# Kernel optimization log

Hardware: AMD Instinct MI355X
Metric: run time of the kernel (lower is better)

## Reference

```python
import jax, jax.numpy as jnp
import numpy as np

B, T, D, H, L, V = 4, 1024, 1024, 16, 12, 8192
DH = D // H
FF = 4 * D


def _ln(x, g, b, eps=1e-5):
    m = x.mean(-1, keepdims=True)
    v = x.var(-1, keepdims=True)
    return (x - m) / jnp.sqrt(v + eps) * g + b


def setup_inputs() -> dict:
    key = jax.random.key(0)
    ks = iter(jax.random.split(key, 32))
    s = 0.02
    inp = {
        "idx": jax.random.randint(next(ks), (B, T), 0, V),
        "tk_emb": jax.random.normal(next(ks), (V, D), jnp.float32) * s,
        "pos_emb": jax.random.normal(next(ks), (V, D), jnp.float32) * s,
        "ln1_g": jnp.ones((L, D)), "ln1_b": jnp.zeros((L, D)),
        "Wq": jax.random.normal(next(ks), (L, H, D, DH), jnp.float32) * s,
        "bq": jnp.zeros((L, H, DH)),
        "Wk": jax.random.normal(next(ks), (L, H, D, DH), jnp.float32) * s,
        "bk": jnp.zeros((L, H, DH)),
        "Wv": jax.random.normal(next(ks), (L, H, D, DH), jnp.float32) * s,
        "bv": jnp.zeros((L, H, DH)),
        "Wo": jax.random.normal(next(ks), (L, D, D), jnp.float32) * s,
        "bo": jnp.zeros((L, D)),
        "ln2_g": jnp.ones((L, D)), "ln2_b": jnp.zeros((L, D)),
        "W1": jax.random.normal(next(ks), (L, D, FF), jnp.float32) * s,
        "b1": jnp.zeros((L, FF)),
        "W2": jax.random.normal(next(ks), (L, FF, D), jnp.float32) * s,
        "b2": jnp.zeros((L, D)),
        "lnf_g": jnp.ones((D,)), "lnf_b": jnp.zeros((D,)),
        "Wout": jax.random.normal(next(ks), (D, V), jnp.float32) * s,
        "bout": jnp.zeros((V,)),
    }
    return inp


def reference(idx, tk_emb, pos_emb, ln1_g, ln1_b, Wq, bq, Wk, bk, Wv, bv,
              Wo, bo, ln2_g, ln2_b, W1, b1, W2, b2, lnf_g, lnf_b, Wout, bout):
    b, t = idx.shape
    x = tk_emb[idx] + pos_emb[:t][None]          # [B,T,D]
    causal = jnp.tril(jnp.ones((t, t), bool))    # [T,T]
    scale = 1.0 / jnp.sqrt(jnp.asarray(DH, x.dtype))

    def block(x, p):
        g1, b1_, wq, bq_, wk, bk_, wv, bv_, wo, bo_, g2, b2_, w1, bb1, w2, bb2 = p
        h = _ln(x, g1, b1_)
        q = jnp.einsum('btd,hde->bhte', h, wq) + bq_[:, None, :]
        k = jnp.einsum('btd,hde->bhte', h, wk) + bk_[:, None, :]
        v = jnp.einsum('btd,hde->bhte', h, wv) + bv_[:, None, :]
        scores = jnp.einsum('bhte,bhse->bhts', q, k) * scale
        scores = jnp.where(causal, scores, jnp.asarray(-jnp.inf, scores.dtype))
        att = jax.nn.softmax(scores, axis=-1)
        o = jnp.einsum('bhts,bhse->bhte', att, v)              # [B,H,T,dh]
        o = o.transpose(0, 2, 1, 3).reshape(x.shape[0], x.shape[1], -1)
        x = x + o @ wo + bo_
        h2 = _ln(x, g2, b2_)
        x = x + jax.nn.gelu(h2 @ w1 + bb1, approximate=False) @ w2 + bb2
        return x, None

    layer_params = (ln1_g, ln1_b, Wq, bq, Wk, bk, Wv, bv, Wo, bo,
                    ln2_g, ln2_b, W1, b1, W2, b2)
    x, _ = jax.lax.scan(block, x, layer_params)
    x = _ln(x, lnf_g, lnf_b)
    logits = x @ Wout + bout
    return logits
```

## Files before the change

### kernel.cpp

```cpp
#include <hip/hip_runtime.h>

#define B_ 4
#define T_ 1024
#define D_ 1024
#define H_ 16
#define DH_ 64
#define L_ 12
#define FF_ 4096
#define V_ 8192
#define M_ 4096

typedef short bf16x8 __attribute__((ext_vector_type(8)));
typedef unsigned short u16x8 __attribute__((ext_vector_type(8)));
typedef unsigned short u16x4 __attribute__((ext_vector_type(4)));
typedef float f32x4 __attribute__((ext_vector_type(4)));

typedef const __attribute__((address_space(1))) void* gas1;
typedef __attribute__((address_space(3))) void* las3;
#define GL2LDS(g, l) __builtin_amdgcn_global_load_lds((gas1)(g), (las3)(l), 16, 0, 0)
#define MFMA16(a, b, c) __builtin_amdgcn_mfma_f32_16x16x32_bf16((a), (b), (c), 0, 0, 0)
#define WVM(n) asm volatile("s_waitcnt vmcnt(" #n ")" ::: "memory")
#define BARRIER() asm volatile("s_barrier" ::: "memory")

static __device__ __forceinline__ unsigned short f2bf(float f) {
  unsigned int u = __builtin_bit_cast(unsigned int, f);
  u += 0x7fffu + ((u >> 16) & 1u);
  return (unsigned short)(u >> 16);
}

__global__ __launch_bounds__(256) void embed_kernel(const int* __restrict__ idx,
                                                    const float* __restrict__ tk,
                                                    const float* __restrict__ pe,
                                                    float* __restrict__ x) {
  const int row = blockIdx.x;
  const int t = row & (T_ - 1);
  const int id = idx[row];
  const int c = threadIdx.x * 4;
  float4 a = *(const float4*)&tk[(size_t)id * D_ + c];
  const float4 p = *(const float4*)&pe[(size_t)t * D_ + c];
  a.x += p.x; a.y += p.y; a.z += p.z; a.w += p.w;
  *(float4*)&x[(size_t)row * D_ + c] = a;
}

__global__ __launch_bounds__(256) void ln_kernel(const float* __restrict__ x,
                                                 const float* __restrict__ g,
                                                 const float* __restrict__ bb,
                                                 unsigned short* __restrict__ out) {
  __shared__ float red[8];
  const int row = blockIdx.x, tid = threadIdx.x;
  const float4 v = *(const float4*)&x[(size_t)row * D_ + tid * 4];
  float s = v.x + v.y + v.z + v.w;
  float s2 = v.x * v.x + v.y * v.y + v.z * v.z + v.w * v.w;
#pragma unroll
  for (int off = 32; off; off >>= 1) {
    s += __shfl_down(s, off);
    s2 += __shfl_down(s2, off);
  }
  if ((tid & 63) == 0) { red[tid >> 6] = s; red[4 + (tid >> 6)] = s2; }
  __syncthreads();
  const float ts = red[0] + red[1] + red[2] + red[3];
  const float ts2 = red[4] + red[5] + red[6] + red[7];
  const float mean = ts * (1.f / 1024.f);
  const float var = ts2 * (1.f / 1024.f) - mean * mean;
  const float rstd = rsqrtf(var + 1e-5f);
  const int c = tid * 4;
  u16x4 ov;
  ov[0] = f2bf((v.x - mean) * rstd * g[c] + bb[c]);
  ov[1] = f2bf((v.y - mean) * rstd * g[c + 1] + bb[c + 1]);
  ov[2] = f2bf((v.z - mean) * rstd * g[c + 2] + bb[c + 2]);
  ov[3] = f2bf((v.w - mean) * rstd * g[c + 3] + bb[c + 3]);
  *(u16x4*)&out[(size_t)row * D_ + c] = ov;
}

__global__ __launch_bounds__(256) void tpose_kernel(const float* __restrict__ in,
                                                    unsigned short* __restrict__ out,
                                                    int R, int C, long in_bs,
                                                    long out_bs_i, int inner, long out_bs_o) {
  __shared__ float tile[32][33];
  const int z = blockIdx.z;
  in += (long)z * in_bs;
  out += (long)(z % inner) * out_bs_i + (long)(z / inner) * out_bs_o;
  const int tx = threadIdx.x, ty = threadIdx.y;
  const int c = blockIdx.x * 32 + tx;
  const int r = blockIdx.y * 32 + ty;
#pragma unroll
  for (int i = 0; i < 4; i++) tile[ty + i * 8][tx] = in[(long)(r + i * 8) * C + c];
  __syncthreads();
  const int oc = blockIdx.y * 32 + tx;
  const int orr = blockIdx.x * 32 + ty;
#pragma unroll
  for (int i = 0; i < 4; i++) out[(long)(orr + i * 8) * R + oc] = f2bf(tile[tx][ty + i * 8]);
}

__global__ void bcat_kernel(const float* __restrict__ bq, const float* __restrict__ bk,
                            const float* __restrict__ bv, float* __restrict__ bqkv) {
  const int l = blockIdx.x;
  for (int i = threadIdx.x; i < 1024; i += 256) {
    bqkv[l * 3072 + i] = bq[l * 1024 + i];
    bqkv[l * 3072 + 1024 + i] = bk[l * 1024 + i];
    bqkv[l * 3072 + 2048 + i] = bv[l * 1024 + i];
  }
}

__global__ __launch_bounds__(256) void redk_kernel(const float* __restrict__ part,
                                                   const float* __restrict__ bias,
                                                   float* __restrict__ x, int N) {
  const size_t i = ((size_t)blockIdx.x * 256 + threadIdx.x) * 4;
  const int col = (int)(i & (size_t)(N - 1));
  float4 r = *(const float4*)&x[i];
  const float4 bv = *(const float4*)&bias[col];
  const size_t stride = (size_t)M_ * N;
  float4 p0 = *(const float4*)&part[i];
  float4 p1 = *(const float4*)&part[i + stride];
  float4 p2 = *(const float4*)&part[i + 2 * stride];
  float4 p3 = *(const float4*)&part[i + 3 * stride];
  r.x += bv.x + ((p0.x + p1.x) + (p2.x + p3.x));
  r.y += bv.y + ((p0.y + p1.y) + (p2.y + p3.y));
  r.z += bv.z + ((p0.z + p1.z) + (p2.z + p3.z));
  r.w += bv.w + ((p0.w + p1.w) + (p2.w + p3.w));
  *(float4*)&x[i] = r;
}

template <int EPI>
__global__ __launch_bounds__(512, 2) void gemm256(const unsigned short* __restrict__ A,
                                                  const unsigned short* __restrict__ Bt,
                                                  const float* __restrict__ bias,
                                                  void* outp, int Kc, int ld, int N) {
  __shared__ unsigned short lds[65536];
  const int tid = threadIdx.x;
  const int lane = tid & 63, w = tid >> 6;
  const int wm = w >> 2, wn = w & 3;
  const int l15 = lane & 15, lh = lane >> 4;
  const int row0 = blockIdx.y * 256, col0 = blockIdx.x * 256;
  const int z = blockIdx.z;
  const int nt = Kc >> 6;
  const int laneoff = (lh * 8) ^ (((l15 >> 1) & 3) << 3);
  const int cswz = ((tid & 3) * 8) ^ (((tid >> 3) & 3) << 3);
  const unsigned short* gA = A + (size_t)(row0 + (tid >> 2)) * ld + z * Kc + cswz;
  const unsigned short* gB = Bt + (size_t)(col0 + (tid >> 2)) * ld + z * Kc + cswz;
  const size_t rblk = (size_t)128 * ld;
  const int arow = wm * 128 + l15;
  const int brow = wn * 64 + l15;

  f32x4 acc[8][4];
#pragma unroll
  for (int m = 0; m < 8; m++)
#pragma unroll
    for (int n = 0; n < 4; n++) acc[m][n] = f32x4{0.f, 0.f, 0.f, 0.f};

  auto issueA = [&](int t, int r) {
    unsigned short* d = lds + (t & 1) * 32768 + r * 8192 + tid * 8;
    const unsigned short* s = gA + t * 64 + r * 32;
    GL2LDS(s, d);
    GL2LDS(s + rblk, d + 4096);
  };
  auto issueB = [&](int t, int r) {
    unsigned short* d = lds + (t & 1) * 32768 + 16384 + r * 8192 + tid * 8;
    const unsigned short* s = gB + t * 64 + r * 32;
    GL2LDS(s, d);
    GL2LDS(s + rblk, d + 4096);
  };

  issueA(0, 0); issueB(0, 0); issueA(0, 1); issueB(0, 1);
  issueA(1, 0); issueB(1, 0);
  WVM(8);
  BARRIER();

  bf16x8 aF[4], bF[4];
  for (int t = 0; t < nt; ++t) {
    const bool last = (t == nt - 1);
    const unsigned short* ab = lds + (t & 1) * 32768;
    const unsigned short* bb2 = ab + 16384;
#pragma unroll
    for (int m = 0; m < 4; m++) aF[m] = *(const bf16x8*)(ab + (arow + m * 16) * 32 + laneoff);
#pragma unroll
    for (int n = 0; n < 4; n++) bF[n] = *(const bf16x8*)(bb2 + (brow + n * 16) * 32 + laneoff);
    if (!last) issueA(t + 1, 1);
    BARRIER();
    __builtin_amdgcn_s_setprio(1);
#pragma unroll
    for (int m = 0; m < 4; m++)
#pragma unroll
      for (int n = 0; n < 4; n++) acc[m][n] = MFMA16(aF[m], bF[n], acc[m][n]);
    __builtin_amdgcn_s_setprio(0);
    BARRIER();
#pragma unroll
    for (int m = 0; m < 4; m++) aF[m] = *(const bf16x8*)(ab + (arow + (m + 4) * 16) * 32 + laneoff);
    if (!last) issueB(t + 1, 1);
    BARRIER();
    __builtin_amdgcn_s_setprio(1);
#pragma unroll
    for (int m = 0; m < 4; m++)
#pragma unroll
      for (int n = 0; n < 4; n++) acc[m + 4][n] = MFMA16(aF[m], bF[n], acc[m + 4][n]);
    __builtin_amdgcn_s_setprio(0);
    if (last) { WVM(0); } else { WVM(8); }
    BARRIER();
#pragma unroll
    for (int m = 0; m < 4; m++) aF[m] = *(const bf16x8*)(ab + 8192 + (arow + m * 16) * 32 + laneoff);
#pragma unroll
    for (int n = 0; n < 4; n++) bF[n] = *(const bf16x8*)(bb2 + 8192 + (brow + n * 16) * 32 + laneoff);
    if (t + 2 < nt) issueA(t + 2, 0);
    BARRIER();
    __builtin_amdgcn_s_setprio(1);
#pragma unroll
    for (int m = 0; m < 4; m++)
#pragma unroll
      for (int n = 0; n < 4; n++) acc[m][n] = MFMA16(aF[m], bF[n], acc[m][n]);
    __builtin_amdgcn_s_setprio(0);
    BARRIER();
#pragma unroll
    for (int m = 0; m < 4; m++) aF[m] = *(const bf16x8*)(ab + 8192 + (arow + (m + 4) * 16) * 32 + laneoff);
    if (t + 2 < nt) issueB(t + 2, 0);
    BARRIER();
    __builtin_amdgcn_s_setprio(1);
#pragma unroll
    for (int m = 0; m < 4; m++)
#pragma unroll
      for (int n = 0; n < 4; n++) acc[m + 4][n] = MFMA16(aF[m], bF[n], acc[m + 4][n]);
    __builtin_amdgcn_s_setprio(0);
    if (!last) {
      if (t == nt - 2) { WVM(4); } else { WVM(8); }
    }
    BARRIER();
  }

#pragma unroll
  for (int n = 0; n < 4; n++) {
    const int c = col0 + wn * 64 + n * 16 + l15;
    const float bv = (EPI == 4) ? 0.f : bias[c];
#pragma unroll
    for (int m = 0; m < 8; m++) {
      const int r = row0 + wm * 128 + m * 16 + lh * 4;
#pragma unroll
      for (int j = 0; j < 4; j++) {
        float val = acc[m][n][j] + bv;
        const size_t oi = (size_t)(r + j) * N + c;
        if constexpr (EPI == 0) {
          ((unsigned short*)outp)[oi] = f2bf(val);
        } else if constexpr (EPI == 1) {
          val = 0.5f * val * (1.f + erff(val * 0.70710678118654752f));
          ((unsigned short*)outp)[oi] = f2bf(val);
        } else if constexpr (EPI == 4) {
          ((float*)outp)[(size_t)z * ((size_t)gridDim.y * 256) * N + oi] = val;
        } else {
          ((float*)outp)[oi] = val;
        }
      }
    }
  }
}

template <int EPI, int BN, int DEPTH>
__global__ __launch_bounds__(256) void gemmP(const unsigned short* __restrict__ A,
                                             const unsigned short* __restrict__ Bt,
                                             const float* __restrict__ bias,
                                             const float* resid, void* outp,
                                             int K, int N) {
  constexpr int NB = DEPTH + 1;
  constexpr int TILE = (128 + BN) * 32;
  constexpr int NF = BN / 32;
  __shared__ unsigned short lds[NB * TILE];
  const int tid = threadIdx.x;
  const int lane = tid & 63;
  const int w = tid >> 6;
  const int l15 = lane & 15, lh = lane >> 4;
  const int wr = (w >> 1) * 64, wc = (w & 1) * (BN / 2);
  const int row0 = blockIdx.y * 128, col0 = blockIdx.x * BN;

  const unsigned short* gA = A + (size_t)(row0 + (tid >> 2)) * K + (tid & 3) * 8;
  const unsigned short* gB = Bt + (size_t)(col0 + (tid >> 2)) * K + (tid & 3) * 8;
  const size_t rstep = (size_t)64 * K;

  f32x4 acc[4][NF];
#pragma unroll
  for (int m = 0; m < 4; m++)
#pragma unroll
    for (int n = 0; n < NF; n++) acc[m][n] = f32x4{0.f, 0.f, 0.f, 0.f};

  const int nt = K >> 5;

  auto ISSUE = [&](int t) {
    unsigned short* buf = lds + (t % NB) * TILE;
    const unsigned short* a = gA + t * 32;
    GL2LDS(a, buf + tid * 8);
    GL2LDS(a + rstep, buf + 2048 + tid * 8);
    const unsigned short* b = gB + t * 32;
    unsigned short* bb = buf + 128 * 32;
    GL2LDS(b, bb + tid * 8);
    if constexpr (BN == 128) GL2LDS(b + rstep, bb + 2048 + tid * 8);
  };

#pragma unroll
  for (int t = 0; t < DEPTH; t++) ISSUE(t);

  for (int i = 0; i < nt; i++) {
    const int rem = nt - 1 - i;
    if (rem >= DEPTH - 1) {
      if constexpr ((2 + (BN == 128 ? 2 : 1)) * (DEPTH - 1) == 4) WVM(4);
      else WVM(6);
    } else if (DEPTH == 3 && rem == 1) {
      WVM(3);
    } else {
      WVM(0);
    }
    BARRIER();
    const unsigned short* buf = lds + (i % NB) * TILE;
    const unsigned short* rdA = buf + (wr + l15) * 32 + lh * 8;
    const unsigned short* rdB = buf + 128 * 32 + (wc + l15) * 32 + lh * 8;
    bf16x8 aF[4], bF[NF];
#pragma unroll
    for (int m = 0; m < 4; m++) aF[m] = *(const bf16x8*)(rdA + m * 512);
#pragma unroll
    for (int n = 0; n < NF; n++) bF[n] = *(const bf16x8*)(rdB + n * 512);
#pragma unroll
    for (int m = 0; m < 4; m++)
#pragma unroll
      for (int n = 0; n < NF; n++) acc[m][n] = MFMA16(aF[m], bF[n], acc[m][n]);
    if (i + DEPTH < nt) ISSUE(i + DEPTH);
  }

#pragma unroll
  for (int n = 0; n < NF; n++) {
    const int c = col0 + wc + n * 16 + l15;
    const float bv = bias[c];
#pragma unroll
    for (int m = 0; m < 4; m++) {
      const int r = row0 + wr + m * 16 + lh * 4;
#pragma unroll
      for (int j = 0; j < 4; j++) {
        float val = acc[m][n][j] + bv;
        const size_t oi = (size_t)(r + j) * N + c;
        if constexpr (EPI == 0) {
          ((unsigned short*)outp)[oi] = f2bf(val);
        } else if constexpr (EPI == 1) {
          val = 0.5f * val * (1.f + erff(val * 0.70710678118654752f));
          ((unsigned short*)outp)[oi] = f2bf(val);
        } else if constexpr (EPI == 2) {
          ((float*)outp)[oi] = resid[oi] + val;
        } else {
          ((float*)outp)[oi] = val;
        }
      }
    }
  }
}

__global__ __launch_bounds__(256) void attn_kernel(const unsigned short* __restrict__ qkv,
                                                   unsigned short* __restrict__ o) {
  __shared__ unsigned short Ks[64 * 72];
  __shared__ unsigned short Vts[64 * 72];
  __shared__ unsigned short Ps[4][16 * 72];
  const int tid = threadIdx.x;
  const int lane = tid & 63, w = tid >> 6;
  const int l15 = lane & 15, lh = lane >> 4;
  const int qt = blockIdx.x;
  const int bh = blockIdx.y;
  const int b = bh >> 4, h = bh & 15;
  const int rb = b * T_;
  const int q0 = qt * 64;

  bf16x8 qf[2];
  {
    const unsigned short* qp = qkv + (size_t)(rb + q0 + w * 16 + l15) * 3072 + h * 64 + lh * 8;
    qf[0] = *(const bf16x8*)qp;
    qf[1] = *(const bf16x8*)(qp + 32);
  }
  f32x4 oa[4];
  float mrun[4], lrun[4];
#pragma unroll
  for (int n = 0; n < 4; n++) oa[n] = f32x4{0.f, 0.f, 0.f, 0.f};
#pragma unroll
  for (int j = 0; j < 4; j++) { mrun[j] = -1e30f; lrun[j] = 0.f; }

  const int row_l = w * 16 + lh * 4;

  for (int kt = 0; kt <= qt; ++kt) {
    __syncthreads();
#pragma unroll
    for (int p = 0; p < 2; p++) {
      const int cc = tid + p * 256;
      const int s = cc >> 3, e8 = (cc & 7) * 8;
      *(u16x8*)&Ks[s * 72 + e8] =
          *(const u16x8*)(qkv + (size_t)(rb + kt * 64 + s) * 3072 + 1024 + h * 64 + e8);
    }
    {
      const unsigned short* vp =
          qkv + (size_t)(rb + kt * 64 + lane) * 3072 + 2048 + h * 64 + w * 16;
      const u16x8 v0 = *(const u16x8*)vp;
      const u16x8 v1 = *(const u16x8*)(vp + 8);
#pragma unroll
      for (int j = 0; j < 8; j++) Vts[(w * 16 + j) * 72 + lane] = v0[j];
#pragma unroll
      for (int j = 0; j < 8; j++) Vts[(w * 16 + 8 + j) * 72 + lane] = v1[j];
    }
    __syncthreads();

    f32x4 sa[4];
#pragma unroll
    for (int n = 0; n < 4; n++) sa[n] = f32x4{0.f, 0.f, 0.f, 0.f};
#pragma unroll
    for (int ke = 0; ke < 2; ke++) {
#pragma unroll
      for (int n = 0; n < 4; n++) {
        const bf16x8 kf = *(const bf16x8*)&Ks[(n * 16 + l15) * 72 + ke * 32 + lh * 8];
        sa[n] = MFMA16(qf[ke], kf, sa[n]);
      }
    }
    float sv[4][4];
    const bool diag = (kt == qt);
#pragma unroll
    for (int n = 0; n < 4; n++) {
      const int colv = kt * 64 + n * 16 + l15;
#pragma unroll
      for (int j = 0; j < 4; j++) {
        float v = sa[n][j] * 0.125f;
        if (diag && colv > q0 + row_l + j) v = -1e30f;
        sv[n][j] = v;
      }
    }
    float mx[4];
#pragma unroll
    for (int j = 0; j < 4; j++)
      mx[j] = fmaxf(fmaxf(sv[0][j], sv[1][j]), fmaxf(sv[2][j], sv[3][j]));
#pragma unroll
    for (int off = 1; off < 16; off <<= 1)
#pragma unroll
      for (int j = 0; j < 4; j++) mx[j] = fmaxf(mx[j], __shfl_xor(mx[j], off));
    float corr[4], rs[4];
#pragma unroll
    for (int j = 0; j < 4; j++) {
      const float m2 = fmaxf(mrun[j], mx[j]);
      corr[j] = __expf(mrun[j] - m2);
      mrun[j] = m2;
      rs[j] = 0.f;
    }
#pragma unroll
    for (int n = 0; n < 4; n++)
#pragma unroll
      for (int j = 0; j < 4; j++) {
        const float p = __expf(sv[n][j] - mrun[j]);
        rs[j] += p;
        Ps[w][(lh * 4 + j) * 72 + n * 16 + l15] = f2bf(p);
      }
#pragma unroll
    for (int off = 1; off < 16; off <<= 1)
#pragma unroll
      for (int j = 0; j < 4; j++) rs[j] += __shfl_xor(rs[j], off);
#pragma unroll
    for (int j = 0; j < 4; j++) lrun[j] = lrun[j] * corr[j] + rs[j];
#pragma unroll
    for (int n = 0; n < 4; n++)
#pragma unroll
      for (int j = 0; j < 4; j++) oa[n][j] *= corr[j];
#pragma unroll
    for (int ks = 0; ks < 2; ks++) {
      const bf16x8 pf = *(const bf16x8*)&Ps[w][l15 * 72 + ks * 32 + lh * 8];
#pragma unroll
      for (int n = 0; n < 4; n++) {
        const bf16x8 vf = *(const bf16x8*)&Vts[(n * 16 + l15) * 72 + ks * 32 + lh * 8];
        oa[n] = MFMA16(pf, vf, oa[n]);
      }
    }
  }
#pragma unroll
  for (int n = 0; n < 4; n++)
#pragma unroll
    for (int j = 0; j < 4; j++) {
      o[(size_t)(rb + q0 + row_l + j) * D_ + h * 64 + n * 16 + l15] =
          f2bf(oa[n][j] / lrun[j]);
    }
}

extern "C" void kernel_launch(void* const* d_in, const int* in_sizes, int n_in,
                              void* d_out, int out_size, void* d_ws, size_t ws_size,
                              hipStream_t stream) {
  const int* idx = (const int*)d_in[0];
  const float* tk = (const float*)d_in[1];
  const float* pe = (const float*)d_in[2];
  const float* ln1g = (const float*)d_in[3];
  const float* ln1b = (const float*)d_in[4];
  const float* Wq = (const float*)d_in[5];
  const float* bq = (const float*)d_in[6];
  const float* Wk = (const float*)d_in[7];
  const float* bk = (const float*)d_in[8];
  const float* Wv = (const float*)d_in[9];
  const float* bv = (const float*)d_in[10];
  const float* Wo = (const float*)d_in[11];
  const float* bo = (const float*)d_in[12];
  const float* ln2g = (const float*)d_in[13];
  const float* ln2b = (const float*)d_in[14];
  const float* W1 = (const float*)d_in[15];
  const float* b1 = (const float*)d_in[16];
  const float* W2 = (const float*)d_in[17];
  const float* b2 = (const float*)d_in[18];
  const float* lnfg = (const float*)d_in[19];
  const float* lnfb = (const float*)d_in[20];
  const float* Wout = (const float*)d_in[21];
  const float* bout = (const float*)d_in[22];

  char* ws = (char*)d_ws;
  size_t off = 0;
  auto alloc = [&](size_t bytes) {
    void* p = ws + off;
    off += (bytes + 255) & ~(size_t)255;
    return p;
  };
  unsigned short* wqkv = (unsigned short*)alloc(12ull * 3072 * 1024 * 2);
  unsigned short* wo = (unsigned short*)alloc(12ull * 1024 * 1024 * 2);
  unsigned short* w1 = (unsigned short*)alloc(12ull * 4096 * 1024 * 2);
  unsigned short* w2 = (unsigned short*)alloc(12ull * 4096 * 1024 * 2);
  unsigned short* wout = (unsigned short*)alloc(8192ull * 1024 * 2);
  float* bqkv = (float*)alloc(12ull * 3072 * 4);
  float* x = (float*)alloc(4096ull * 1024 * 4);
  unsigned short* hb = (unsigned short*)alloc(4096ull * 1024 * 2);
  unsigned short* qkvb = (unsigned short*)alloc(4096ull * 3072 * 2);
  unsigned short* ob = (unsigned short*)alloc(4096ull * 1024 * 2);
  unsigned short* ub = (unsigned short*)alloc(4096ull * 4096 * 2);
  float* part = (float*)alloc(4ull * 4096 * 1024 * 4);

  const dim3 tb(32, 8);
  tpose_kernel<<<dim3(2, 32, 192), tb, 0, stream>>>(Wq, wqkv, 1024, 64, 65536, 65536, 16, 3145728);
  tpose_kernel<<<dim3(2, 32, 192), tb, 0, stream>>>(Wk, wqkv + 1024 * 1024, 1024, 64, 65536, 65536, 16, 3145728);
  tpose_kernel<<<dim3(2, 32, 192), tb, 0, stream>>>(Wv, wqkv + 2048 * 1024, 1024, 64, 65536, 65536, 16, 3145728);
  tpose_kernel<<<dim3(32, 32, 12), tb, 0, stream>>>(Wo, wo, 1024, 1024, 1048576, 0, 1, 1048576);
  tpose_kernel<<<dim3(128, 32, 12), tb, 0, stream>>>(W1, w1, 1024, 4096, 4194304, 0, 1, 4194304);
  tpose_kernel<<<dim3(32, 128, 12), tb, 0, stream>>>(W2, w2, 4096, 1024, 4194304, 0, 1, 4194304);
  tpose_kernel<<<dim3(256, 32, 1), tb, 0, stream>>>(Wout, wout, 1024, 8192, 0, 0, 1, 0);
  bcat_kernel<<<12, 256, 0, stream>>>(bq, bk, bv, bqkv);
  embed_kernel<<<4096, 256, 0, stream>>>(idx, tk, pe, x);

  for (int l = 0; l < 12; l++) {
    ln_kernel<<<4096, 256, 0, stream>>>(x, ln1g + l * 1024, ln1b + l * 1024, hb);
    gemmP<0, 128, 2><<<dim3(24, 32), 256, 0, stream>>>(hb, wqkv + (size_t)l * 3145728,
                                                       bqkv + l * 3072, nullptr, qkvb, 1024, 3072);
    attn_kernel<<<dim3(16, 64), 256, 0, stream>>>(qkvb, ob);
    gemmP<2, 64, 3><<<dim3(16, 32), 256, 0, stream>>>(ob, wo + (size_t)l * 1048576,
                                                      bo + l * 1024, x, x, 1024, 1024);
    ln_kernel<<<4096, 256, 0, stream>>>(x, ln2g + l * 1024, ln2b + l * 1024, hb);
    gemm256<1><<<dim3(16, 16), 512, 0, stream>>>(hb, w1 + (size_t)l * 4194304,
                                                 b1 + l * 4096, ub, 1024, 1024, 4096);
    gemm256<4><<<dim3(4, 16, 4), 512, 0, stream>>>(ub, w2 + (size_t)l * 4194304,
                                                   nullptr, part, 1024, 4096, 1024);
    redk_kernel<<<4096, 256, 0, stream>>>(part, b2 + l * 1024, x, 1024);
  }
  ln_kernel<<<4096, 256, 0, stream>>>(x, lnfg, lnfb, hb);
  gemm256<3><<<dim3(32, 16), 512, 0, stream>>>(hb, wout, bout, d_out, 1024, 1024, 8192);
}
```

Baseline: 3.608 ms.

## Double-buffer attention K/V tiles with 128-row query blocks and larger transpose tiles

The attention kernel now uses 512 threads covering 128 query rows per block. K/V tiles are double-buffered in shared memory, with the next tile's global loads held in registers and issued during compute, so each iteration needs only one barrier. s_setprio is raised around the MFMA sections. The weight-transpose kernel moves to 64x64 tiles with 64x4 threads. The larger query block halves the grid and may cut occupancy, and the diagonal masking now spans two key tiles per query block.

```diff
diff --git a/kernel.cpp b/kernel.cpp
--- a/kernel.cpp
+++ b/kernel.cpp
@@ -20,6 +20,7 @@
 #define GL2LDS(g, l) __builtin_amdgcn_global_load_lds((gas1)(g), (las3)(l), 16, 0, 0)
 #define MFMA16(a, b, c) __builtin_amdgcn_mfma_f32_16x16x32_bf16((a), (b), (c), 0, 0, 0)
 #define WVM(n) asm volatile("s_waitcnt vmcnt(" #n ")" ::: "memory")
+#define WLG() asm volatile("s_waitcnt lgkmcnt(0)" ::: "memory")
 #define BARRIER() asm volatile("s_barrier" ::: "memory")
 
 static __device__ __forceinline__ unsigned short f2bf(float f) {
@@ -76,20 +77,21 @@
                                                     unsigned short* __restrict__ out,
                                                     int R, int C, long in_bs,
                                                     long out_bs_i, int inner, long out_bs_o) {
-  __shared__ float tile[32][33];
+  __shared__ float tile[64][65];
   const int z = blockIdx.z;
   in += (long)z * in_bs;
   out += (long)(z % inner) * out_bs_i + (long)(z / inner) * out_bs_o;
   const int tx = threadIdx.x, ty = threadIdx.y;
-  const int c = blockIdx.x * 32 + tx;
-  const int r = blockIdx.y * 32 + ty;
-#pragma unroll
-  for (int i = 0; i < 4; i++) tile[ty + i * 8][tx] = in[(long)(r + i * 8) * C + c];
+  const int c = blockIdx.x * 64 + tx;
+  const int r0 = blockIdx.y * 64;
+#pragma unroll
+  for (int i = 0; i < 16; i++) tile[ty + i * 4][tx] = in[(long)(r0 + ty + i * 4) * C + c];
   __syncthreads();
-  const int oc = blockIdx.y * 32 + tx;
-  const int orr = blockIdx.x * 32 + ty;
-#pragma unroll
-  for (int i = 0; i < 4; i++) out[(long)(orr + i * 8) * R + oc] = f2bf(tile[tx][ty + i * 8]);
+  const int oc = blockIdx.y * 64 + tx;
+  const int or0 = blockIdx.x * 64;
+#pragma unroll
+  for (int i = 0; i < 16; i++)
+    out[(long)(or0 + ty + i * 4) * R + oc] = f2bf(tile[tx][ty + i * 4]);
 }
 
 __global__ void bcat_kernel(const float* __restrict__ bq, const float* __restrict__ bk,
@@ -346,11 +348,11 @@
   }
 }
 
-__global__ __launch_bounds__(256) void attn_kernel(const unsigned short* __restrict__ qkv,
+__global__ __launch_bounds__(512) void attn_kernel(const unsigned short* __restrict__ qkv,
                                                    unsigned short* __restrict__ o) {
-  __shared__ unsigned short Ks[64 * 72];
-  __shared__ unsigned short Vts[64 * 72];
-  __shared__ unsigned short Ps[4][16 * 72];
+  __shared__ unsigned short Ks[2][64 * 72];
+  __shared__ unsigned short Vts[2][64 * 72];
+  __shared__ unsigned short Ps[8][16 * 72];
   const int tid = threadIdx.x;
   const int lane = tid & 63, w = tid >> 6;
   const int l15 = lane & 15, lh = lane >> 4;
@@ -358,7 +360,8 @@
   const int bh = blockIdx.y;
   const int b = bh >> 4, h = bh & 15;
   const int rb = b * T_;
-  const int q0 = qt * 64;
+  const int q0 = qt * 128;
+  const int nkt = 2 * qt + 2;
 
   bf16x8 qf[2];
   {
@@ -375,40 +378,43 @@
 
   const int row_l = w * 16 + lh * 4;
 
-  for (int kt = 0; kt <= qt; ++kt) {
-    __syncthreads();
-#pragma unroll
-    for (int p = 0; p < 2; p++) {
-      const int cc = tid + p * 256;
-      const int s = cc >> 3, e8 = (cc & 7) * 8;
-      *(u16x8*)&Ks[s * 72 + e8] =
-          *(const u16x8*)(qkv + (size_t)(rb + kt * 64 + s) * 3072 + 1024 + h * 64 + e8);
-    }
-    {
-      const unsigned short* vp =
-          qkv + (size_t)(rb + kt * 64 + lane) * 3072 + 2048 + h * 64 + w * 16;
-      const u16x8 v0 = *(const u16x8*)vp;
-      const u16x8 v1 = *(const u16x8*)(vp + 8);
-#pragma unroll
-      for (int j = 0; j < 8; j++) Vts[(w * 16 + j) * 72 + lane] = v0[j];
-#pragma unroll
-      for (int j = 0; j < 8; j++) Vts[(w * 16 + 8 + j) * 72 + lane] = v1[j];
-    }
-    __syncthreads();
-
+  u16x8 kreg, vreg;
+  auto loadKV = [&](int kt) {
+    kreg = *(const u16x8*)(qkv + (size_t)(rb + kt * 64 + (tid >> 3)) * 3072 + 1024 + h * 64 +
+                           (tid & 7) * 8);
+    vreg = *(const u16x8*)(qkv + (size_t)(rb + kt * 64 + lane) * 3072 + 2048 + h * 64 + w * 8);
+  };
+  auto writeKV = [&](int kt) {
+    const int bs = kt & 1;
+    *(u16x8*)&Ks[bs][(tid >> 3) * 72 + (tid & 7) * 8] = kreg;
+#pragma unroll
+    for (int j = 0; j < 8; j++) Vts[bs][(w * 8 + j) * 72 + lane] = vreg[j];
+  };
+
+  loadKV(0);
+  WVM(0);
+  writeKV(0);
+  loadKV(1);
+  WLG();
+  BARRIER();
+
+  for (int kt = 0; kt < nkt; ++kt) {
+    const int bs = kt & 1;
     f32x4 sa[4];
 #pragma unroll
     for (int n = 0; n < 4; n++) sa[n] = f32x4{0.f, 0.f, 0.f, 0.f};
+    __builtin_amdgcn_s_setprio(1);
 #pragma unroll
     for (int ke = 0; ke < 2; ke++) {
 #pragma unroll
       for (int n = 0; n < 4; n++) {
-        const bf16x8 kf = *(const bf16x8*)&Ks[(n * 16 + l15) * 72 + ke * 32 + lh * 8];
+        const bf16x8 kf = *(const bf16x8*)&Ks[bs][(n * 16 + l15) * 72 + ke * 32 + lh * 8];
         sa[n] = MFMA16(qf[ke], kf, sa[n]);
       }
     }
+    __builtin_amdgcn_s_setprio(0);
     float sv[4][4];
-    const bool diag = (kt == qt);
+    const bool diag = (kt >= 2 * qt);
 #pragma unroll
     for (int n = 0; n < 4; n++) {
       const int colv = kt * 64 + n * 16 + l15;
@@ -453,14 +459,23 @@
     for (int n = 0; n < 4; n++)
 #pragma unroll
       for (int j = 0; j < 4; j++) oa[n][j] *= corr[j];
+    __builtin_amdgcn_s_setprio(1);
 #pragma unroll
     for (int ks = 0; ks < 2; ks++) {
       const bf16x8 pf = *(const bf16x8*)&Ps[w][l15 * 72 + ks * 32 + lh * 8];
 #pragma unroll
       for (int n = 0; n < 4; n++) {
-        const bf16x8 vf = *(const bf16x8*)&Vts[(n * 16 + l15) * 72 + ks * 32 + lh * 8];
+        const bf16x8 vf = *(const bf16x8*)&Vts[bs][(n * 16 + l15) * 72 + ks * 32 + lh * 8];
         oa[n] = MFMA16(pf, vf, oa[n]);
       }
+    }
+    __builtin_amdgcn_s_setprio(0);
+    if (kt + 1 < nkt) {
+      WVM(0);
+      writeKV(kt + 1);
+      if (kt + 2 < nkt) loadKV(kt + 2);
+      WLG();
+      BARRIER();
     }
   }
 #pragma unroll
@@ -519,14 +534,14 @@
   unsigned short* ub = (unsigned short*)alloc(4096ull * 4096 * 2);
   float* part = (float*)alloc(4ull * 4096 * 1024 * 4);
 
-  const dim3 tb(32, 8);
-  tpose_kernel<<<dim3(2, 32, 192), tb, 0, stream>>>(Wq, wqkv, 1024, 64, 65536, 65536, 16, 3145728);
-  tpose_kernel<<<dim3(2, 32, 192), tb, 0, stream>>>(Wk, wqkv + 1024 * 1024, 1024, 64, 65536, 65536, 16, 3145728);
-  tpose_kernel<<<dim3(2, 32, 192), tb, 0, stream>>>(Wv, wqkv + 2048 * 1024, 1024, 64, 65536, 65536, 16, 3145728);
-  tpose_kernel<<<dim3(32, 32, 12), tb, 0, stream>>>(Wo, wo, 1024, 1024, 1048576, 0, 1, 1048576);
-  tpose_kernel<<<dim3(128, 32, 12), tb, 0, stream>>>(W1, w1, 1024, 4096, 4194304, 0, 1, 4194304);
-  tpose_kernel<<<dim3(32, 128, 12), tb, 0, stream>>>(W2, w2, 4096, 1024, 4194304, 0, 1, 4194304);
-  tpose_kernel<<<dim3(256, 32, 1), tb, 0, stream>>>(Wout, wout, 1024, 8192, 0, 0, 1, 0);
+  const dim3 tb(64, 4);
+  tpose_kernel<<<dim3(1, 16, 192), tb, 0, stream>>>(Wq, wqkv, 1024, 64, 65536, 65536, 16, 3145728);
+  tpose_kernel<<<dim3(1, 16, 192), tb, 0, stream>>>(Wk, wqkv + 1024 * 1024, 1024, 64, 65536, 65536, 16, 3145728);
+  tpose_kernel<<<dim3(1, 16, 192), tb, 0, stream>>>(Wv, wqkv + 2048 * 1024, 1024, 64, 65536, 65536, 16, 3145728);
+  tpose_kernel<<<dim3(16, 16, 12), tb, 0, stream>>>(Wo, wo, 1024, 1024, 1048576, 0, 1, 1048576);
+  tpose_kernel<<<dim3(64, 16, 12), tb, 0, stream>>>(W1, w1, 1024, 4096, 4194304, 0, 1, 4194304);
+  tpose_kernel<<<dim3(16, 64, 12), tb, 0, stream>>>(W2, w2, 4096, 1024, 4194304, 0, 1, 4194304);
+  tpose_kernel<<<dim3(128, 16, 1), tb, 0, stream>>>(Wout, wout, 1024, 8192, 0, 0, 1, 0);
   bcat_kernel<<<12, 256, 0, stream>>>(bq, bk, bv, bqkv);
   embed_kernel<<<4096, 256, 0, stream>>>(idx, tk, pe, x);
 
@@ -534,7 +549,7 @@
     ln_kernel<<<4096, 256, 0, stream>>>(x, ln1g + l * 1024, ln1b + l * 1024, hb);
     gemmP<0, 128, 2><<<dim3(24, 32), 256, 0, stream>>>(hb, wqkv + (size_t)l * 3145728,
                                                        bqkv + l * 3072, nullptr, qkvb, 1024, 3072);
-    attn_kernel<<<dim3(16, 64), 256, 0, stream>>>(qkvb, ob);
+    attn_kernel<<<dim3(8, 64), 512, 0, stream>>>(qkvb, ob);
     gemmP<2, 64, 3><<<dim3(16, 32), 256, 0, stream>>>(ob, wo + (size_t)l * 1048576,
                                                       bo + l * 1024, x, x, 1024, 1024);
     ln_kernel<<<4096, 256, 0, stream>>>(x, ln2g + l * 1024, ln2b + l * 1024, hb);
```

New measurement: 3.193 ms. 11.5% less time.
